# Optimization experiments

Hardware: AMD Instinct MI355X
Metric: run time of the kernel (lower is better)

## Reference

```python
import jax, jax.numpy as jnp
from jax import lax
import numpy as np

K = 2        # k-hop MIS / number of rw SpGEMM iterations
EPS = 0.5    # lazy random-walk epsilon
N = 2048     # nodes
D = 512      # feature dim
E = 65536    # edges (avg degree 32)


def setup_inputs() -> dict:
    key = jax.random.key(0)
    k1, k2, k3, k4 = jax.random.split(key, 4)
    edge_index = jax.random.randint(k1, (2, E), 0, N, dtype=jnp.int32)
    edge_attr = jax.random.uniform(k2, (E,), dtype=jnp.float32)
    x = jax.random.normal(k3, (N, D), dtype=jnp.float32)
    rank = jnp.arange(N, dtype=jnp.int32)  # node ordering ('random' ordering = some permutation; identity here)
    u = jax.random.uniform(k4, (N, N), dtype=jnp.float32)  # noise for row-wise multinomial sampling
    return {"edge_index": edge_index, "edge_attr": edge_attr, "x": x, "rank": rank, "u": u}


def _maximal_k_independent_set(row, col, rank, n, k):
    """Greedy maximal k-independent set: nodes that are local rank-minima within k hops."""
    big = jnp.int32(n)

    def prop_min(r):  # one hop of min-propagation (message row -> col), keep self
        return jnp.minimum(jax.ops.segment_min(r[row], col, num_segments=n), r)

    def prop_or(b):   # one hop of boolean OR propagation (as int32)
        return jnp.maximum(jax.ops.segment_max(b[row], col, num_segments=n), b)

    def cond(st):
        mis, mask, mr = st
        return ~jnp.all(mask)

    def body(st):
        mis, mask, mr = st
        for _ in range(k):
            mr = prop_min(mr)
        mis = mis | (rank == mr)
        mk = mis.astype(jnp.int32)
        for _ in range(k):
            mk = prop_or(mk)
        mask = mk > 0
        mr = jnp.where(mask, big, rank)
        return mis, mask, mr

    init = (jnp.zeros(n, bool), jnp.zeros(n, bool), rank)
    mis, _, _ = lax.while_loop(cond, body, init)
    return mis


def _row_normalize(m):
    s = m.sum(axis=1, keepdims=True)
    return m / jnp.where(s > 0, s, 1.0)


def reference(edge_index, edge_attr, x, rank, u):
    n = x.shape[0]
    row, col = edge_index[0], edge_index[1]

    # --- MIS over the graph structure (integer-only) ---
    mis = _maximal_k_independent_set(row, col, rank, n, K)

    # --- adjacency (dense padded form of the SparseTensor) ---
    adj = jnp.zeros((n, n), x.dtype).at[row, col].add(edge_attr)

    # --- lazy random walk: rw = D^-1 A, offdiag *= (1-eps), diag = old_diag + eps ---
    rw = _row_normalize(adj)
    di = jnp.arange(n)
    new_diag = rw[di, di] + EPS  # computed BEFORE scaling, per original code
    rw = (rw * (1.0 - EPS)).at[di, di].set(new_diag)

    # --- c_mat = rw^K @ eye[:, mis]; padded to [n, n] with zero non-MIS columns ---
    c = jnp.where(mis[None, :], jnp.eye(n, dtype=x.dtype), 0.0)
    for _ in range(K):
        c = rw @ c
    c = _row_normalize(c)

    # --- sample_partition_matrix: per-row multinomial via Gumbel-argmax ---
    g = -jnp.log(-jnp.log(u + 1e-20) + 1e-20)
    logits = jnp.where(c > 0, jnp.log(jnp.maximum(c, 1e-30)), -jnp.inf) + g
    cluster = jnp.argmax(logits, axis=1)                 # [n] cluster id (a MIS column)
    c_hard = jax.nn.one_hot(cluster, n, dtype=x.dtype)   # partition matrix [n, n]

    # --- p_inv = row-normalized c_hard.T ---
    counts = c_hard.sum(axis=0)
    p_inv = c_hard.T / jnp.where(counts > 0, counts, 1.0)[:, None]

    # --- coarsen: c^T A c, pool: p_inv @ x ---
    adj_c = c_hard.T @ adj @ c_hard
    x_pool = p_inv @ x
    return adj_c, c_hard, p_inv, mis, x_pool
```

## Files before the change

kernel.cpp:

```cpp
#include <hip/hip_runtime.h>
#include <hip/hip_bf16.h>
#include <math.h>
#include <stdint.h>

#define NN 2048
#define DD 512
#define EE 65536
#define EPSV 0.5f
#define SEN 2048

static const size_t SZ = (size_t)NN * NN;

__global__ __launch_bounds__(256) void build_adj(const int* __restrict__ row,
                                                 const int* __restrict__ col,
                                                 const float* __restrict__ attr,
                                                 float* __restrict__ adj,
                                                 float* __restrict__ rowsum,
                                                 int* __restrict__ degree,
                                                 int* __restrict__ cdeg) {
  int e = blockIdx.x * 256 + threadIdx.x;
  float a = attr[e];
  int r = row[e], c = col[e];
  atomicAdd(&adj[r * NN + c], a);
  atomicAdd(&rowsum[r], a);
  atomicAdd(&degree[r], 1);
  atomicAdd(&cdeg[c], 1);
}

__global__ __launch_bounds__(1024) void csr_scan_pad(const int* __restrict__ degree,
                                                     const int* __restrict__ cdeg,
                                                     int* __restrict__ row_ptr,
                                                     int* __restrict__ fill_ptr,
                                                     int* __restrict__ col_ptr,
                                                     int* __restrict__ cfill_ptr,
                                                     unsigned short* __restrict__ colidx,
                                                     unsigned short* __restrict__ rowidx) {
  __shared__ int a[NN], b[NN], c[NN], d[NN];
  int t = threadIdx.x;
  for (int v = t; v < NN; v += 1024) {
    a[v] = (degree[v] + 15) & ~15;
    c[v] = (cdeg[v] + 15) & ~15;
  }
  __syncthreads();
  int* s1 = a; int* d1 = b; int* s2 = c; int* d2 = d;
  for (int off = 1; off < NN; off <<= 1) {
    for (int v = t; v < NN; v += 1024) {
      d1[v] = s1[v] + (v >= off ? s1[v - off] : 0);
      d2[v] = s2[v] + (v >= off ? s2[v - off] : 0);
    }
    __syncthreads();
    int* tp = s1; s1 = d1; d1 = tp;
    tp = s2; s2 = d2; d2 = tp;
  }
  for (int v = t; v < NN; v += 1024) {
    int dg = degree[v];
    int end = s1[v];
    int excl = end - ((dg + 15) & ~15);
    row_ptr[v] = excl;
    fill_ptr[v] = excl;
    for (int e = excl + dg; e < end; ++e) colidx[e] = (unsigned short)v;
    dg = cdeg[v];
    end = s2[v];
    excl = end - ((dg + 15) & ~15);
    col_ptr[v] = excl;
    cfill_ptr[v] = excl;
    for (int e = excl + dg; e < end; ++e) rowidx[e] = (unsigned short)v;
  }
  if (t == 0) {
    row_ptr[NN] = s1[NN - 1];
    col_ptr[NN] = s2[NN - 1];
  }
}

__global__ __launch_bounds__(256) void csr_fill(const int* __restrict__ row,
                                                const int* __restrict__ col,
                                                int* __restrict__ fill_ptr,
                                                int* __restrict__ cfill_ptr,
                                                unsigned short* __restrict__ colidx,
                                                unsigned short* __restrict__ rowidx) {
  int e = blockIdx.x * 256 + threadIdx.x;
  int r = row[e], c = col[e];
  colidx[atomicAdd(&fill_ptr[r], 1)] = (unsigned short)c;
  rowidx[atomicAdd(&cfill_ptr[c], 1)] = (unsigned short)r;
}

__global__ __launch_bounds__(1024) void mis_kernel(const int* __restrict__ row_ptr_g,
                                                   const int* __restrict__ col_ptr_g,
                                                   const unsigned short* __restrict__ colidx,
                                                   const unsigned short* __restrict__ rowidx,
                                                   const int* __restrict__ rank_g,
                                                   int* __restrict__ mis_flag,
                                                   int* __restrict__ mis_list,
                                                   int* __restrict__ misinv,
                                                   int* __restrict__ mis_count) {
  __shared__ int rank_s[NN];
  __shared__ int mr[NN];
  __shared__ int cov[NN];
  __shared__ int dly[NN];
  __shared__ int mis_s[NN];
  __shared__ int row_ptr_s[NN + 1];
  __shared__ int col_ptr_s[NN + 1];
  __shared__ int unc[2][NN];
  __shared__ int dl[NN];
  __shared__ int ucnt[2];
  __shared__ int dcnt;
  __shared__ int cnt;
  int t = threadIdx.x;
  const uint4* col4 = (const uint4*)colidx;
  const uint4* row4 = (const uint4*)rowidx;

  for (int v = t; v < NN; v += 1024) {
    int rk = rank_g[v];
    rank_s[v] = rk;
    mr[v] = rk;
    cov[v] = 0;
    dly[v] = 0;
    mis_s[v] = 0;
    row_ptr_s[v] = row_ptr_g[v];
    col_ptr_s[v] = col_ptr_g[v];
    unc[0][v] = v;
  }
  if (t == 0) {
    row_ptr_s[NN] = row_ptr_g[NN];
    col_ptr_s[NN] = col_ptr_g[NN];
    ucnt[0] = NN;
    ucnt[1] = 0;
    dcnt = 0;
    cnt = 0;
  }
  __syncthreads();

  int cur = 0;
  for (int round = 0; round < NN; ++round) {
    int U = ucnt[cur];
    if (round) {
      for (int v = t; v < NN; v += 1024) {
        mr[v] = cov[v] ? SEN : rank_s[v];
        dly[v] = 0;
      }
      if (t == 0) { ucnt[cur ^ 1] = 0; dcnt = 0; }
      __syncthreads();
    }
    for (int i = t; i < U; i += 1024) {
      int v = unc[cur][i];
      int val = rank_s[v];
      int e0 = row_ptr_s[v];
      int nch = (row_ptr_s[v + 1] - e0) >> 3;
      const uint4* b4 = col4 + (e0 >> 3);
      for (int cI = 0; cI < nch; cI += 2) {
        uint4 A = b4[cI], B = b4[cI + 1];
        atomicMin(&mr[A.x & 0xFFFFu], val); atomicMin(&mr[A.x >> 16], val);
        atomicMin(&mr[A.y & 0xFFFFu], val); atomicMin(&mr[A.y >> 16], val);
        atomicMin(&mr[A.z & 0xFFFFu], val); atomicMin(&mr[A.z >> 16], val);
        atomicMin(&mr[A.w & 0xFFFFu], val); atomicMin(&mr[A.w >> 16], val);
        atomicMin(&mr[B.x & 0xFFFFu], val); atomicMin(&mr[B.x >> 16], val);
        atomicMin(&mr[B.y & 0xFFFFu], val); atomicMin(&mr[B.y >> 16], val);
        atomicMin(&mr[B.z & 0xFFFFu], val); atomicMin(&mr[B.z >> 16], val);
        atomicMin(&mr[B.w & 0xFFFFu], val); atomicMin(&mr[B.w >> 16], val);
      }
    }
    __syncthreads();
    for (int i = t; i < U; i += 1024) {
      int v = unc[cur][i];
      int val = mr[v];
      int e0 = col_ptr_s[v];
      int nch = (col_ptr_s[v + 1] - e0) >> 3;
      const uint4* b4 = row4 + (e0 >> 3);
      for (int cI = 0; cI < nch; cI += 2) {
        uint4 A = b4[cI], B = b4[cI + 1];
        int m0 = min(mr[A.x & 0xFFFFu], mr[A.x >> 16]);
        int m1 = min(mr[A.y & 0xFFFFu], mr[A.y >> 16]);
        int m2 = min(mr[A.z & 0xFFFFu], mr[A.z >> 16]);
        int m3 = min(mr[A.w & 0xFFFFu], mr[A.w >> 16]);
        int m4 = min(mr[B.x & 0xFFFFu], mr[B.x >> 16]);
        int m5 = min(mr[B.y & 0xFFFFu], mr[B.y >> 16]);
        int m6 = min(mr[B.z & 0xFFFFu], mr[B.z >> 16]);
        int m7 = min(mr[B.w & 0xFFFFu], mr[B.w >> 16]);
        val = min(val, min(min(min(m0, m1), min(m2, m3)),
                           min(min(m4, m5), min(m6, m7))));
      }
      if (rank_s[v] == val) {
        mis_s[v] = 1;
        dly[v] = 1;
        dl[atomicAdd(&dcnt, 1)] = v;
      }
    }
    __syncthreads();
    int D = dcnt;
    for (int i = t; i < D; i += 1024) {
      int v = dl[i];
      int e0 = row_ptr_s[v];
      int nch = (row_ptr_s[v + 1] - e0) >> 3;
      const uint4* b4 = col4 + (e0 >> 3);
      for (int cI = 0; cI < nch; cI += 2) {
        uint4 A = b4[cI], B = b4[cI + 1];
        dly[A.x & 0xFFFFu] = 1; dly[A.x >> 16] = 1;
        dly[A.y & 0xFFFFu] = 1; dly[A.y >> 16] = 1;
        dly[A.z & 0xFFFFu] = 1; dly[A.z >> 16] = 1;
        dly[A.w & 0xFFFFu] = 1; dly[A.w >> 16] = 1;
        dly[B.x & 0xFFFFu] = 1; dly[B.x >> 16] = 1;
        dly[B.y & 0xFFFFu] = 1; dly[B.y >> 16] = 1;
        dly[B.z & 0xFFFFu] = 1; dly[B.z >> 16] = 1;
        dly[B.w & 0xFFFFu] = 1; dly[B.w >> 16] = 1;
      }
    }
    __syncthreads();
    for (int i = t; i < U; i += 1024) {
      int v = unc[cur][i];
      int c1 = dly[v];
      if (!c1) {
        int e0 = col_ptr_s[v];
        int nch = (col_ptr_s[v + 1] - e0) >> 3;
        const uint4* b4 = row4 + (e0 >> 3);
        for (int cI = 0; cI < nch; cI += 2) {
          uint4 A = b4[cI], B = b4[cI + 1];
          c1 |= dly[A.x & 0xFFFFu] | dly[A.x >> 16] |
                dly[A.y & 0xFFFFu] | dly[A.y >> 16] |
                dly[A.z & 0xFFFFu] | dly[A.z >> 16] |
                dly[A.w & 0xFFFFu] | dly[A.w >> 16] |
                dly[B.x & 0xFFFFu] | dly[B.x >> 16] |
                dly[B.y & 0xFFFFu] | dly[B.y >> 16] |
                dly[B.z & 0xFFFFu] | dly[B.z >> 16] |
                dly[B.w & 0xFFFFu] | dly[B.w >> 16];
          if (c1) break;
        }
      }
      if (c1) cov[v] = 1;
      else unc[cur ^ 1][atomicAdd(&ucnt[cur ^ 1], 1)] = v;
    }
    __syncthreads();
    if (ucnt[cur ^ 1] == 0) break;
    cur ^= 1;
  }

  for (int v = t; v < NN; v += 1024) {
    int s = mis_s[v];
    mis_flag[v] = s;
    int slot = -1;
    if (s) {
      slot = atomicAdd(&cnt, 1);
      mis_list[slot] = v;
    }
    misinv[v] = slot;
  }
  __syncthreads();
  if (t == 0) *mis_count = cnt;
}

__global__ __launch_bounds__(256) void rw_transform_gather(float* __restrict__ adj,
                                                           const float* __restrict__ rowsum,
                                                           const int* __restrict__ misinv,
                                                           float* __restrict__ Bc) {
  int idx = blockIdx.x * 256 + threadIdx.x;
  int i = idx >> 11, j = idx & (NN - 1);
  float s = rowsum[i];
  s = (s > 0.f) ? s : 1.f;
  float v = adj[idx] / s;
  v = (i == j) ? (v + EPSV) : (v * (1.f - EPSV));
  adj[idx] = v;
  int tc = misinv[j];
  if (tc >= 0) Bc[(size_t)tc * NN + i] = v;
}

__device__ inline unsigned int f32_key(float x) {
  unsigned int u = __float_as_uint(x);
  return (u & 0x80000000u) ? ~u : (u | 0x80000000u);
}
__device__ inline float dot4(float4 a, float4 b) {
  return ((a.x * b.x + a.y * b.y) + (a.z * b.z + a.w * b.w));
}
__device__ inline unsigned long long umax64(unsigned long long a, unsigned long long b) {
  return a > b ? a : b;
}

__global__ __launch_bounds__(256) void c2_argmax(const float* __restrict__ rw,
                                                 const float* __restrict__ Bc,
                                                 const float* __restrict__ u,
                                                 const int* __restrict__ mis_list,
                                                 const int* __restrict__ mis_count,
                                                 unsigned long long* __restrict__ packed) {
  int M = *mis_count;
  int ncg = (M + 3) >> 2;
  int njobs = ncg * 64;
  int lane = threadIdx.x & 63, w = threadIdx.x >> 6;
  for (int j = blockIdx.x; j < njobs; j += gridDim.x) {
    int cg = j >> 6, tile = j & 63;
    int c0 = cg * 4;
    float4 creg[4][8];
    int mcol[4];
#pragma unroll
    for (int cc = 0; cc < 4; ++cc) {
      int colv = c0 + cc;
      int cl = colv < M ? colv : (M - 1);
      mcol[cc] = mis_list[cl];
      const float4* cb = (const float4*)(Bc + (size_t)cl * NN);
#pragma unroll
      for (int q = 0; q < 8; ++q) creg[cc][q] = cb[q * 64 + lane];
    }
    int rbase = tile * 32 + w * 8;
#pragma unroll
    for (int it = 0; it < 8; ++it) {
      int r = rbase + it;
      const float4* rp = (const float4*)(rw + (size_t)r * NN);
      float4 a0 = rp[lane], a1 = rp[64 + lane], a2 = rp[128 + lane], a3 = rp[192 + lane];
      float4 a4 = rp[256 + lane], a5 = rp[320 + lane], a6 = rp[384 + lane], a7 = rp[448 + lane];
      float sacc[4];
#pragma unroll
      for (int cc = 0; cc < 4; ++cc) {
        float s01 = dot4(a0, creg[cc][0]) + dot4(a1, creg[cc][1]);
        float s23 = dot4(a2, creg[cc][2]) + dot4(a3, creg[cc][3]);
        float s45 = dot4(a4, creg[cc][4]) + dot4(a5, creg[cc][5]);
        float s67 = dot4(a6, creg[cc][6]) + dot4(a7, creg[cc][7]);
        float s = (s01 + s23) + (s45 + s67);
        s += __shfl_xor(s, 32);
        s += __shfl_xor(s, 16);
        s += __shfl_xor(s, 8);
        s += __shfl_xor(s, 4);
        s += __shfl_xor(s, 2);
        s += __shfl_xor(s, 1);
        sacc[cc] = s;
      }
      if (lane == 0) {
        unsigned long long best = 0ull;
#pragma unroll
        for (int cc = 0; cc < 4; ++cc) {
          if (c0 + cc < M && sacc[cc] > 0.f) {
            int m = mcol[cc];
            float uu = u[(size_t)r * NN + m];
            float g = -logf(-logf(uu + 1e-20f) + 1e-20f);
            float logit = logf(sacc[cc]) + g;
            unsigned long long key =
                ((unsigned long long)f32_key(logit) << 32) | (unsigned int)(NN - 1 - m);
            best = umax64(best, key);
          }
        }
        if (best) atomicMax(&packed[r], best);
      }
    }
  }
}

__global__ __launch_bounds__(256) void cluster_decode(const unsigned long long* __restrict__ packed,
                                                      int* __restrict__ cluster,
                                                      int* __restrict__ counts) {
  int i = blockIdx.x * 256 + threadIdx.x;
  unsigned long long p = packed[i];
  int m = (p == 0ull) ? 0 : (NN - 1 - (int)(p & 0xFFFFFFFFull));
  cluster[i] = m;
  atomicAdd(&counts[m], 1);
}

__global__ __launch_bounds__(256) void scatter_fused(const int* __restrict__ row,
                                                     const int* __restrict__ col,
                                                     const float* __restrict__ attr,
                                                     const float* __restrict__ x,
                                                     const int* __restrict__ cluster,
                                                     float* __restrict__ adjc,
                                                     float* __restrict__ xp) {
  int idx = blockIdx.x * 256 + threadIdx.x;
  if (idx < EE) {
    int cr = cluster[row[idx]], cc = cluster[col[idx]];
    atomicAdd(&adjc[(size_t)cr * NN + cc], attr[idx]);
  }
  int i = idx >> 9;
  atomicAdd(&xp[cluster[i] * DD + (idx & (DD - 1))], x[idx]);
}

__global__ __launch_bounds__(256) void write_chpm(const int* __restrict__ cluster,
                                                  const int* __restrict__ counts,
                                                  const int* __restrict__ mis_flag,
                                                  float* __restrict__ out_ch,
                                                  float* __restrict__ out_pinv,
                                                  float* __restrict__ out_mis,
                                                  float* __restrict__ out_xp) {
  int idx = blockIdx.x * 256 + threadIdx.x;
  int a = idx >> 11, b = idx & (NN - 1);
  out_ch[idx] = (cluster[a] == b) ? 1.f : 0.f;
  float pv = 0.f;
  if (cluster[b] == a) {
    int c = counts[a];
    pv = 1.f / (float)(c > 0 ? c : 1);
  }
  out_pinv[idx] = pv;
  if (idx < NN) out_mis[idx] = mis_flag[idx] ? 1.f : 0.f;
  if (idx < NN * DD) {
    int c = counts[idx >> 9];
    out_xp[idx] = out_xp[idx] / (float)(c > 0 ? c : 1);
  }
}

extern "C" void kernel_launch(void* const* d_in, const int* in_sizes, int n_in,
                              void* d_out, int out_size, void* d_ws, size_t ws_size,
                              hipStream_t stream) {
  const int*   edge_index = (const int*)d_in[0];
  const float* edge_attr  = (const float*)d_in[1];
  const float* x          = (const float*)d_in[2];
  const int*   rank       = (const int*)d_in[3];
  const float* u          = (const float*)d_in[4];
  float* out              = (float*)d_out;

  const int* row = edge_index;
  const int* col = edge_index + EE;

  float* out_adjc = out;
  float* out_ch   = out + SZ;
  float* out_pinv = out + 2 * SZ;
  float* out_mis  = out + 3 * SZ;
  float* out_xp   = out + 3 * SZ + NN;

  unsigned long long* packed = (unsigned long long*)d_ws;
  float* rowsum    = (float*)(packed + NN);
  int*   counts    = (int*)(rowsum + NN);
  int*   degree    = counts + NN;
  int*   cdeg      = degree + NN;
  int*   mis_flag  = cdeg + NN;
  int*   cluster   = mis_flag + NN;
  int*   mis_list  = cluster + NN;
  int*   misinv    = mis_list + NN;
  int*   mis_count = misinv + NN;
  int*   fill_ptr  = mis_count + 1;
  int*   cfill_ptr = fill_ptr + NN;
  int*   row_ptr   = cfill_ptr + NN;
  int*   col_ptr   = row_ptr + NN + 1;
  unsigned short* colidx =
      (unsigned short*)(((uintptr_t)(col_ptr + NN + 1) + 31) & ~(uintptr_t)31);
  unsigned short* rowidx = colidx + 98304;

  hipMemsetAsync(out_adjc, 0, SZ * sizeof(float), stream);
  hipMemsetAsync(out_xp, 0, (size_t)NN * DD * sizeof(float), stream);
  hipMemsetAsync(d_ws, 0, NN * sizeof(unsigned long long) + 4 * NN * sizeof(int), stream);

  build_adj<<<EE / 256, 256, 0, stream>>>(row, col, edge_attr, out_adjc, rowsum, degree, cdeg);
  csr_scan_pad<<<1, 1024, 0, stream>>>(degree, cdeg, row_ptr, fill_ptr, col_ptr, cfill_ptr,
                                       colidx, rowidx);
  csr_fill<<<EE / 256, 256, 0, stream>>>(row, col, fill_ptr, cfill_ptr, colidx, rowidx);
  mis_kernel<<<1, 1024, 0, stream>>>(row_ptr, col_ptr, colidx, rowidx, rank,
                                     mis_flag, mis_list, misinv, mis_count);
  rw_transform_gather<<<(NN * NN) / 256, 256, 0, stream>>>(out_adjc, rowsum, misinv, out_ch);
  c2_argmax<<<1024, 256, 0, stream>>>(out_adjc, out_ch, u, mis_list, mis_count, packed);
  cluster_decode<<<NN / 256, 256, 0, stream>>>(packed, cluster, counts);

  hipMemsetAsync(out_adjc, 0, SZ * sizeof(float), stream);
  scatter_fused<<<(NN * DD) / 256, 256, 0, stream>>>(row, col, edge_attr, x, cluster,
                                                     out_adjc, out_xp);

  write_chpm<<<(NN * NN) / 256, 256, 0, stream>>>(cluster, counts, mis_flag,
                                                  out_ch, out_pinv, out_mis, out_xp);
}
```

Measured before the change: 265.2 us.

## Fuse CSR construction into MIS kernel and fold small launches into neighbors

Moves degree counting, rowsum, prefix scan and CSR fill into the single-block MIS kernel using shared-memory atomics, which drops the csr_scan_pad and csr_fill launches and two memsets. The mark-neighbors step is merged into the MIS-detection loop, removing a barrier and the dl list. cluster_decode is folded into scatter_fused, and the x_pool zeroing moves into rw_transform_gather. The cost is that the edge scatter now runs on one 1024-thread workgroup instead of the whole GPU, and the kernel needs a 64-entry per-thread register array.

```diff
diff --git a/kernel.cpp b/kernel.cpp
--- a/kernel.cpp
+++ b/kernel.cpp
@@ -8,91 +8,26 @@
 #define EE 65536
 #define EPSV 0.5f
 #define SEN 2048
+#define PADE 98304
 
 static const size_t SZ = (size_t)NN * NN;
 
 __global__ __launch_bounds__(256) void build_adj(const int* __restrict__ row,
                                                  const int* __restrict__ col,
                                                  const float* __restrict__ attr,
-                                                 float* __restrict__ adj,
-                                                 float* __restrict__ rowsum,
-                                                 int* __restrict__ degree,
-                                                 int* __restrict__ cdeg) {
+                                                 float* __restrict__ adj) {
   int e = blockIdx.x * 256 + threadIdx.x;
-  float a = attr[e];
-  int r = row[e], c = col[e];
-  atomicAdd(&adj[r * NN + c], a);
-  atomicAdd(&rowsum[r], a);
-  atomicAdd(&degree[r], 1);
-  atomicAdd(&cdeg[c], 1);
-}
-
-__global__ __launch_bounds__(1024) void csr_scan_pad(const int* __restrict__ degree,
-                                                     const int* __restrict__ cdeg,
-                                                     int* __restrict__ row_ptr,
-                                                     int* __restrict__ fill_ptr,
-                                                     int* __restrict__ col_ptr,
-                                                     int* __restrict__ cfill_ptr,
-                                                     unsigned short* __restrict__ colidx,
-                                                     unsigned short* __restrict__ rowidx) {
-  __shared__ int a[NN], b[NN], c[NN], d[NN];
-  int t = threadIdx.x;
-  for (int v = t; v < NN; v += 1024) {
-    a[v] = (degree[v] + 15) & ~15;
-    c[v] = (cdeg[v] + 15) & ~15;
-  }
-  __syncthreads();
-  int* s1 = a; int* d1 = b; int* s2 = c; int* d2 = d;
-  for (int off = 1; off < NN; off <<= 1) {
-    for (int v = t; v < NN; v += 1024) {
-      d1[v] = s1[v] + (v >= off ? s1[v - off] : 0);
-      d2[v] = s2[v] + (v >= off ? s2[v - off] : 0);
-    }
-    __syncthreads();
-    int* tp = s1; s1 = d1; d1 = tp;
-    tp = s2; s2 = d2; d2 = tp;
-  }
-  for (int v = t; v < NN; v += 1024) {
-    int dg = degree[v];
-    int end = s1[v];
-    int excl = end - ((dg + 15) & ~15);
-    row_ptr[v] = excl;
-    fill_ptr[v] = excl;
-    for (int e = excl + dg; e < end; ++e) colidx[e] = (unsigned short)v;
-    dg = cdeg[v];
-    end = s2[v];
-    excl = end - ((dg + 15) & ~15);
-    col_ptr[v] = excl;
-    cfill_ptr[v] = excl;
-    for (int e = excl + dg; e < end; ++e) rowidx[e] = (unsigned short)v;
-  }
-  if (t == 0) {
-    row_ptr[NN] = s1[NN - 1];
-    col_ptr[NN] = s2[NN - 1];
-  }
-}
-
-__global__ __launch_bounds__(256) void csr_fill(const int* __restrict__ row,
-                                                const int* __restrict__ col,
-                                                int* __restrict__ fill_ptr,
-                                                int* __restrict__ cfill_ptr,
-                                                unsigned short* __restrict__ colidx,
-                                                unsigned short* __restrict__ rowidx) {
-  int e = blockIdx.x * 256 + threadIdx.x;
-  int r = row[e], c = col[e];
-  colidx[atomicAdd(&fill_ptr[r], 1)] = (unsigned short)c;
-  rowidx[atomicAdd(&cfill_ptr[c], 1)] = (unsigned short)r;
-}
-
-__global__ __launch_bounds__(1024) void mis_kernel(const int* __restrict__ row_ptr_g,
-                                                   const int* __restrict__ col_ptr_g,
-                                                   const unsigned short* __restrict__ colidx,
-                                                   const unsigned short* __restrict__ rowidx,
-                                                   const int* __restrict__ rank_g,
-                                                   int* __restrict__ mis_flag,
-                                                   int* __restrict__ mis_list,
-                                                   int* __restrict__ misinv,
-                                                   int* __restrict__ mis_count) {
+  atomicAdd(&adj[row[e] * NN + col[e]], attr[e]);
+}
+
+__global__ __launch_bounds__(1024) void fused_mis(
+    const int* __restrict__ row, const int* __restrict__ col,
+    const float* __restrict__ attr, const int* __restrict__ rank_g,
+    unsigned short* __restrict__ colidx, unsigned short* __restrict__ rowidx,
+    float* __restrict__ rowsum_g, unsigned long long* __restrict__ packed,
+    int* __restrict__ counts, int* __restrict__ mis_flag,
+    int* __restrict__ mis_list, int* __restrict__ misinv,
+    int* __restrict__ mis_count) {
   __shared__ int rank_s[NN];
   __shared__ int mr[NN];
   __shared__ int cov[NN];
@@ -101,13 +36,77 @@
   __shared__ int row_ptr_s[NN + 1];
   __shared__ int col_ptr_s[NN + 1];
   __shared__ int unc[2][NN];
-  __shared__ int dl[NN];
   __shared__ int ucnt[2];
-  __shared__ int dcnt;
   __shared__ int cnt;
   int t = threadIdx.x;
-  const uint4* col4 = (const uint4*)colidx;
-  const uint4* row4 = (const uint4*)rowidx;
+  float* rowsum_s = (float*)mis_s;
+
+  for (int v = t; v < NN; v += 1024) {
+    mr[v] = 0;
+    cov[v] = 0;
+    rowsum_s[v] = 0.f;
+  }
+  __syncthreads();
+  unsigned pe[64];
+#pragma unroll
+  for (int i = 0; i < 64; ++i) {
+    int e = t + 1024 * i;
+    int r = row[e], c = col[e];
+    pe[i] = ((unsigned)r << 11) | (unsigned)c;
+    atomicAdd(&mr[r], 1);
+    atomicAdd(&cov[c], 1);
+    atomicAdd(&rowsum_s[r], attr[e]);
+  }
+  __syncthreads();
+
+  int* s1 = dly;    int* d1 = mis_s;
+  int* s2 = unc[0]; int* d2 = unc[1];
+  for (int v = t; v < NN; v += 1024) {
+    rowsum_g[v] = rowsum_s[v];
+    s1[v] = (mr[v] + 15) & ~15;
+    s2[v] = (cov[v] + 15) & ~15;
+  }
+  __syncthreads();
+  for (int off = 1; off < NN; off <<= 1) {
+    for (int v = t; v < NN; v += 1024) {
+      d1[v] = s1[v] + (v >= off ? s1[v - off] : 0);
+      d2[v] = s2[v] + (v >= off ? s2[v - off] : 0);
+    }
+    __syncthreads();
+    int* tp = s1; s1 = d1; d1 = tp;
+    tp = s2; s2 = d2; d2 = tp;
+  }
+  for (int v = t; v < NN; v += 1024) {
+    int end = s1[v];
+    row_ptr_s[v] = end - ((mr[v] + 15) & ~15);
+    end = s2[v];
+    col_ptr_s[v] = end - ((cov[v] + 15) & ~15);
+  }
+  if (t == 0) {
+    row_ptr_s[NN] = s1[NN - 1];
+    col_ptr_s[NN] = s2[NN - 1];
+  }
+  __syncthreads();
+
+  for (int v = t; v < NN; v += 1024) {
+    int e0 = row_ptr_s[v];
+    dly[v] = e0;
+    for (int e = e0 + mr[v]; e < row_ptr_s[v + 1]; ++e)
+      colidx[e] = (unsigned short)v;
+    e0 = col_ptr_s[v];
+    mis_s[v] = e0;
+    for (int e = e0 + cov[v]; e < col_ptr_s[v + 1]; ++e)
+      rowidx[e] = (unsigned short)v;
+  }
+  __syncthreads();
+#pragma unroll
+  for (int i = 0; i < 64; ++i) {
+    unsigned p = pe[i];
+    int r = p >> 11, c = p & 2047;
+    colidx[atomicAdd(&dly[r], 1)] = (unsigned short)c;
+    rowidx[atomicAdd(&mis_s[c], 1)] = (unsigned short)r;
+  }
+  __syncthreads();
 
   for (int v = t; v < NN; v += 1024) {
     int rk = rank_g[v];
@@ -116,19 +115,19 @@
     cov[v] = 0;
     dly[v] = 0;
     mis_s[v] = 0;
-    row_ptr_s[v] = row_ptr_g[v];
-    col_ptr_s[v] = col_ptr_g[v];
     unc[0][v] = v;
+    packed[v] = 0ull;
+    counts[v] = 0;
   }
   if (t == 0) {
-    row_ptr_s[NN] = row_ptr_g[NN];
-    col_ptr_s[NN] = col_ptr_g[NN];
     ucnt[0] = NN;
     ucnt[1] = 0;
-    dcnt = 0;
     cnt = 0;
   }
   __syncthreads();
+
+  const uint4* col4 = (const uint4*)colidx;
+  const uint4* row4 = (const uint4*)rowidx;
 
   int cur = 0;
   for (int round = 0; round < NN; ++round) {
@@ -138,7 +137,7 @@
         mr[v] = cov[v] ? SEN : rank_s[v];
         dly[v] = 0;
       }
-      if (t == 0) { ucnt[cur ^ 1] = 0; dcnt = 0; }
+      if (t == 0) ucnt[cur ^ 1] = 0;
       __syncthreads();
     }
     for (int i = t; i < U; i += 1024) {
@@ -182,26 +181,20 @@
       if (rank_s[v] == val) {
         mis_s[v] = 1;
         dly[v] = 1;
-        dl[atomicAdd(&dcnt, 1)] = v;
-      }
-    }
-    __syncthreads();
-    int D = dcnt;
-    for (int i = t; i < D; i += 1024) {
-      int v = dl[i];
-      int e0 = row_ptr_s[v];
-      int nch = (row_ptr_s[v + 1] - e0) >> 3;
-      const uint4* b4 = col4 + (e0 >> 3);
-      for (int cI = 0; cI < nch; cI += 2) {
-        uint4 A = b4[cI], B = b4[cI + 1];
-        dly[A.x & 0xFFFFu] = 1; dly[A.x >> 16] = 1;
-        dly[A.y & 0xFFFFu] = 1; dly[A.y >> 16] = 1;
-        dly[A.z & 0xFFFFu] = 1; dly[A.z >> 16] = 1;
-        dly[A.w & 0xFFFFu] = 1; dly[A.w >> 16] = 1;
-        dly[B.x & 0xFFFFu] = 1; dly[B.x >> 16] = 1;
-        dly[B.y & 0xFFFFu] = 1; dly[B.y >> 16] = 1;
-        dly[B.z & 0xFFFFu] = 1; dly[B.z >> 16] = 1;
-        dly[B.w & 0xFFFFu] = 1; dly[B.w >> 16] = 1;
+        int f0 = row_ptr_s[v];
+        int fch = (row_ptr_s[v + 1] - f0) >> 3;
+        const uint4* c4 = col4 + (f0 >> 3);
+        for (int cI = 0; cI < fch; cI += 2) {
+          uint4 A = c4[cI], B = c4[cI + 1];
+          dly[A.x & 0xFFFFu] = 1; dly[A.x >> 16] = 1;
+          dly[A.y & 0xFFFFu] = 1; dly[A.y >> 16] = 1;
+          dly[A.z & 0xFFFFu] = 1; dly[A.z >> 16] = 1;
+          dly[A.w & 0xFFFFu] = 1; dly[A.w >> 16] = 1;
+          dly[B.x & 0xFFFFu] = 1; dly[B.x >> 16] = 1;
+          dly[B.y & 0xFFFFu] = 1; dly[B.y >> 16] = 1;
+          dly[B.z & 0xFFFFu] = 1; dly[B.z >> 16] = 1;
+          dly[B.w & 0xFFFFu] = 1; dly[B.w >> 16] = 1;
+        }
       }
     }
     __syncthreads();
@@ -250,7 +243,8 @@
 __global__ __launch_bounds__(256) void rw_transform_gather(float* __restrict__ adj,
                                                            const float* __restrict__ rowsum,
                                                            const int* __restrict__ misinv,
-                                                           float* __restrict__ Bc) {
+                                                           float* __restrict__ Bc,
+                                                           float* __restrict__ out_xp) {
   int idx = blockIdx.x * 256 + threadIdx.x;
   int i = idx >> 11, j = idx & (NN - 1);
   float s = rowsum[i];
@@ -260,6 +254,7 @@
   adj[idx] = v;
   int tc = misinv[j];
   if (tc >= 0) Bc[(size_t)tc * NN + i] = v;
+  if (idx < NN * DD) out_xp[idx] = 0.f;
 }
 
 __device__ inline unsigned int f32_key(float x) {
@@ -271,6 +266,9 @@
 }
 __device__ inline unsigned long long umax64(unsigned long long a, unsigned long long b) {
   return a > b ? a : b;
+}
+__device__ inline int pdecode(unsigned long long p) {
+  return (p == 0ull) ? 0 : (NN - 1 - (int)(p & 0xFFFFFFFFull));
 }
 
 __global__ __launch_bounds__(256) void c2_argmax(const float* __restrict__ rw,
@@ -340,30 +338,28 @@
   }
 }
 
-__global__ __launch_bounds__(256) void cluster_decode(const unsigned long long* __restrict__ packed,
-                                                      int* __restrict__ cluster,
-                                                      int* __restrict__ counts) {
-  int i = blockIdx.x * 256 + threadIdx.x;
-  unsigned long long p = packed[i];
-  int m = (p == 0ull) ? 0 : (NN - 1 - (int)(p & 0xFFFFFFFFull));
-  cluster[i] = m;
-  atomicAdd(&counts[m], 1);
-}
-
 __global__ __launch_bounds__(256) void scatter_fused(const int* __restrict__ row,
                                                      const int* __restrict__ col,
                                                      const float* __restrict__ attr,
                                                      const float* __restrict__ x,
-                                                     const int* __restrict__ cluster,
+                                                     const unsigned long long* __restrict__ packed,
+                                                     int* __restrict__ cluster,
+                                                     int* __restrict__ counts,
                                                      float* __restrict__ adjc,
                                                      float* __restrict__ xp) {
   int idx = blockIdx.x * 256 + threadIdx.x;
+  int i = idx >> 9;
+  int ci = pdecode(packed[i]);
+  if ((idx & 511) == 0) {
+    cluster[i] = ci;
+    atomicAdd(&counts[ci], 1);
+  }
   if (idx < EE) {
-    int cr = cluster[row[idx]], cc = cluster[col[idx]];
+    int cr = pdecode(packed[row[idx]]);
+    int cc = pdecode(packed[col[idx]]);
     atomicAdd(&adjc[(size_t)cr * NN + cc], attr[idx]);
   }
-  int i = idx >> 9;
-  atomicAdd(&xp[cluster[i] * DD + (idx & (DD - 1))], x[idx]);
+  atomicAdd(&xp[ci * DD + (idx & (DD - 1))], x[idx]);
 }
 
 __global__ __launch_bounds__(256) void write_chpm(const int* __restrict__ cluster,
@@ -411,38 +407,27 @@
   unsigned long long* packed = (unsigned long long*)d_ws;
   float* rowsum    = (float*)(packed + NN);
   int*   counts    = (int*)(rowsum + NN);
-  int*   degree    = counts + NN;
-  int*   cdeg      = degree + NN;
-  int*   mis_flag  = cdeg + NN;
+  int*   mis_flag  = counts + NN;
   int*   cluster   = mis_flag + NN;
   int*   mis_list  = cluster + NN;
   int*   misinv    = mis_list + NN;
   int*   mis_count = misinv + NN;
-  int*   fill_ptr  = mis_count + 1;
-  int*   cfill_ptr = fill_ptr + NN;
-  int*   row_ptr   = cfill_ptr + NN;
-  int*   col_ptr   = row_ptr + NN + 1;
   unsigned short* colidx =
-      (unsigned short*)(((uintptr_t)(col_ptr + NN + 1) + 31) & ~(uintptr_t)31);
-  unsigned short* rowidx = colidx + 98304;
+      (unsigned short*)(((uintptr_t)(mis_count + 1) + 31) & ~(uintptr_t)31);
+  unsigned short* rowidx = colidx + PADE;
 
   hipMemsetAsync(out_adjc, 0, SZ * sizeof(float), stream);
-  hipMemsetAsync(out_xp, 0, (size_t)NN * DD * sizeof(float), stream);
-  hipMemsetAsync(d_ws, 0, NN * sizeof(unsigned long long) + 4 * NN * sizeof(int), stream);
-
-  build_adj<<<EE / 256, 256, 0, stream>>>(row, col, edge_attr, out_adjc, rowsum, degree, cdeg);
-  csr_scan_pad<<<1, 1024, 0, stream>>>(degree, cdeg, row_ptr, fill_ptr, col_ptr, cfill_ptr,
-                                       colidx, rowidx);
-  csr_fill<<<EE / 256, 256, 0, stream>>>(row, col, fill_ptr, cfill_ptr, colidx, rowidx);
-  mis_kernel<<<1, 1024, 0, stream>>>(row_ptr, col_ptr, colidx, rowidx, rank,
-                                     mis_flag, mis_list, misinv, mis_count);
-  rw_transform_gather<<<(NN * NN) / 256, 256, 0, stream>>>(out_adjc, rowsum, misinv, out_ch);
+  build_adj<<<EE / 256, 256, 0, stream>>>(row, col, edge_attr, out_adjc);
+  fused_mis<<<1, 1024, 0, stream>>>(row, col, edge_attr, rank, colidx, rowidx,
+                                    rowsum, packed, counts, mis_flag, mis_list,
+                                    misinv, mis_count);
+  rw_transform_gather<<<(NN * NN) / 256, 256, 0, stream>>>(out_adjc, rowsum, misinv,
+                                                           out_ch, out_xp);
   c2_argmax<<<1024, 256, 0, stream>>>(out_adjc, out_ch, u, mis_list, mis_count, packed);
-  cluster_decode<<<NN / 256, 256, 0, stream>>>(packed, cluster, counts);
 
   hipMemsetAsync(out_adjc, 0, SZ * sizeof(float), stream);
-  scatter_fused<<<(NN * DD) / 256, 256, 0, stream>>>(row, col, edge_attr, x, cluster,
-                                                     out_adjc, out_xp);
+  scatter_fused<<<(NN * DD) / 256, 256, 0, stream>>>(row, col, edge_attr, x, packed,
+                                                     cluster, counts, out_adjc, out_xp);
 
   write_chpm<<<(NN * NN) / 256, 256, 0, stream>>>(cluster, counts, mis_flag,
                                                   out_ch, out_pinv, out_mis, out_xp);
```

After: 414.8 us. 1.56x slower.

## Build random-walk rows from CSR and fuse zeroing, decode and scatter kernels

Applied to the files above, without the earlier changes.

The dense adjacency is no longer built with global atomics on a zeroed 16MB buffer. Edge values are stored alongside the CSR column indices, and each row of the random-walk matrix is built in shared memory, then written once. Several memsets and small kernels are merged: the cluster decode is combined with zeroing the output, and the pooled-feature and coarsened-adjacency scatters are folded into the one-hot/p_inv writer, with pooled features divided by cluster counts before the atomic add. This removes two full-matrix memsets and one full-matrix pass, at the cost of shared-memory atomics per row and a changed summation order for x_pool.

```diff
diff --git a/kernel.cpp b/kernel.cpp
--- a/kernel.cpp
+++ b/kernel.cpp
@@ -8,23 +8,17 @@
 #define EE 65536
 #define EPSV 0.5f
 #define SEN 2048
+#define PADE 98304
 
 static const size_t SZ = (size_t)NN * NN;
 
-__global__ __launch_bounds__(256) void build_adj(const int* __restrict__ row,
+__global__ __launch_bounds__(256) void count_deg(const int* __restrict__ row,
                                                  const int* __restrict__ col,
-                                                 const float* __restrict__ attr,
-                                                 float* __restrict__ adj,
-                                                 float* __restrict__ rowsum,
                                                  int* __restrict__ degree,
                                                  int* __restrict__ cdeg) {
   int e = blockIdx.x * 256 + threadIdx.x;
-  float a = attr[e];
-  int r = row[e], c = col[e];
-  atomicAdd(&adj[r * NN + c], a);
-  atomicAdd(&rowsum[r], a);
-  atomicAdd(&degree[r], 1);
-  atomicAdd(&cdeg[c], 1);
+  atomicAdd(&degree[row[e]], 1);
+  atomicAdd(&cdeg[col[e]], 1);
 }
 
 __global__ __launch_bounds__(1024) void csr_scan_pad(const int* __restrict__ degree,
@@ -34,12 +28,17 @@
                                                      int* __restrict__ col_ptr,
                                                      int* __restrict__ cfill_ptr,
                                                      unsigned short* __restrict__ colidx,
-                                                     unsigned short* __restrict__ rowidx) {
+                                                     unsigned short* __restrict__ rowidx,
+                                                     float* __restrict__ avals,
+                                                     unsigned long long* __restrict__ packed,
+                                                     int* __restrict__ counts) {
   __shared__ int a[NN], b[NN], c[NN], d[NN];
   int t = threadIdx.x;
   for (int v = t; v < NN; v += 1024) {
     a[v] = (degree[v] + 15) & ~15;
     c[v] = (cdeg[v] + 15) & ~15;
+    packed[v] = 0ull;
+    counts[v] = 0;
   }
   __syncthreads();
   int* s1 = a; int* d1 = b; int* s2 = c; int* d2 = d;
@@ -58,7 +57,10 @@
     int excl = end - ((dg + 15) & ~15);
     row_ptr[v] = excl;
     fill_ptr[v] = excl;
-    for (int e = excl + dg; e < end; ++e) colidx[e] = (unsigned short)v;
+    for (int e = excl + dg; e < end; ++e) {
+      colidx[e] = (unsigned short)v;
+      avals[e] = 0.f;
+    }
     dg = cdeg[v];
     end = s2[v];
     excl = end - ((dg + 15) & ~15);
@@ -74,13 +76,17 @@
 
 __global__ __launch_bounds__(256) void csr_fill(const int* __restrict__ row,
                                                 const int* __restrict__ col,
+                                                const float* __restrict__ attr,
                                                 int* __restrict__ fill_ptr,
                                                 int* __restrict__ cfill_ptr,
                                                 unsigned short* __restrict__ colidx,
-                                                unsigned short* __restrict__ rowidx) {
+                                                unsigned short* __restrict__ rowidx,
+                                                float* __restrict__ avals) {
   int e = blockIdx.x * 256 + threadIdx.x;
   int r = row[e], c = col[e];
-  colidx[atomicAdd(&fill_ptr[r], 1)] = (unsigned short)c;
+  int pos = atomicAdd(&fill_ptr[r], 1);
+  colidx[pos] = (unsigned short)c;
+  avals[pos] = attr[e];
   rowidx[atomicAdd(&cfill_ptr[c], 1)] = (unsigned short)r;
 }
 
@@ -247,19 +253,38 @@
   if (t == 0) *mis_count = cnt;
 }
 
-__global__ __launch_bounds__(256) void rw_transform_gather(float* __restrict__ adj,
-                                                           const float* __restrict__ rowsum,
-                                                           const int* __restrict__ misinv,
-                                                           float* __restrict__ Bc) {
-  int idx = blockIdx.x * 256 + threadIdx.x;
-  int i = idx >> 11, j = idx & (NN - 1);
-  float s = rowsum[i];
+__global__ __launch_bounds__(256) void rw_build(const int* __restrict__ row_ptr,
+                                                const unsigned short* __restrict__ colidx,
+                                                const float* __restrict__ avals,
+                                                const int* __restrict__ misinv,
+                                                float* __restrict__ rw,
+                                                float* __restrict__ Bc) {
+  int i = blockIdx.x;
+  __shared__ float rowbuf[NN];
+  __shared__ float ssum;
+  int t = threadIdx.x;
+  for (int j = t; j < NN; j += 256) rowbuf[j] = 0.f;
+  if (t == 0) ssum = 0.f;
+  __syncthreads();
+  int e0 = row_ptr[i], e1 = row_ptr[i + 1];
+  float part = 0.f;
+  for (int e = e0 + t; e < e1; e += 256) {
+    float a = avals[e];
+    atomicAdd(&rowbuf[colidx[e]], a);
+    part += a;
+  }
+  for (int off = 32; off; off >>= 1) part += __shfl_down(part, off);
+  if ((t & 63) == 0) atomicAdd(&ssum, part);
+  __syncthreads();
+  float s = ssum;
   s = (s > 0.f) ? s : 1.f;
-  float v = adj[idx] / s;
-  v = (i == j) ? (v + EPSV) : (v * (1.f - EPSV));
-  adj[idx] = v;
-  int tc = misinv[j];
-  if (tc >= 0) Bc[(size_t)tc * NN + i] = v;
+  for (int j = t; j < NN; j += 256) {
+    float v = rowbuf[j] / s;
+    v = (i == j) ? (v + EPSV) : (v * (1.f - EPSV));
+    rw[(size_t)i * NN + j] = v;
+    int tc = misinv[j];
+    if (tc >= 0) Bc[(size_t)tc * NN + i] = v;
+  }
 }
 
 __device__ inline unsigned int f32_key(float x) {
@@ -271,6 +296,9 @@
 }
 __device__ inline unsigned long long umax64(unsigned long long a, unsigned long long b) {
   return a > b ? a : b;
+}
+__device__ inline int pdecode(unsigned long long p) {
+  return (p == 0ull) ? 0 : (NN - 1 - (int)(p & 0xFFFFFFFFull));
 }
 
 __global__ __launch_bounds__(256) void c2_argmax(const float* __restrict__ rw,
@@ -340,39 +368,33 @@
   }
 }
 
-__global__ __launch_bounds__(256) void cluster_decode(const unsigned long long* __restrict__ packed,
-                                                      int* __restrict__ cluster,
-                                                      int* __restrict__ counts) {
-  int i = blockIdx.x * 256 + threadIdx.x;
-  unsigned long long p = packed[i];
-  int m = (p == 0ull) ? 0 : (NN - 1 - (int)(p & 0xFFFFFFFFull));
-  cluster[i] = m;
-  atomicAdd(&counts[m], 1);
-}
-
-__global__ __launch_bounds__(256) void scatter_fused(const int* __restrict__ row,
-                                                     const int* __restrict__ col,
-                                                     const float* __restrict__ attr,
-                                                     const float* __restrict__ x,
-                                                     const int* __restrict__ cluster,
-                                                     float* __restrict__ adjc,
-                                                     float* __restrict__ xp) {
+__global__ __launch_bounds__(256) void decode_zero(const unsigned long long* __restrict__ packed,
+                                                   int* __restrict__ cluster,
+                                                   int* __restrict__ counts,
+                                                   float* __restrict__ adjc,
+                                                   float* __restrict__ xp) {
   int idx = blockIdx.x * 256 + threadIdx.x;
-  if (idx < EE) {
-    int cr = cluster[row[idx]], cc = cluster[col[idx]];
-    atomicAdd(&adjc[(size_t)cr * NN + cc], attr[idx]);
-  }
-  int i = idx >> 9;
-  atomicAdd(&xp[cluster[i] * DD + (idx & (DD - 1))], x[idx]);
-}
-
-__global__ __launch_bounds__(256) void write_chpm(const int* __restrict__ cluster,
-                                                  const int* __restrict__ counts,
-                                                  const int* __restrict__ mis_flag,
-                                                  float* __restrict__ out_ch,
-                                                  float* __restrict__ out_pinv,
-                                                  float* __restrict__ out_mis,
-                                                  float* __restrict__ out_xp) {
+  if (idx < (int)SZ) adjc[idx] = 0.f;
+  else xp[idx - (int)SZ] = 0.f;
+  if (idx < NN) {
+    int m = pdecode(packed[idx]);
+    cluster[idx] = m;
+    atomicAdd(&counts[m], 1);
+  }
+}
+
+__global__ __launch_bounds__(256) void scatter_chpm(const int* __restrict__ row,
+                                                    const int* __restrict__ col,
+                                                    const float* __restrict__ attr,
+                                                    const float* __restrict__ x,
+                                                    const int* __restrict__ cluster,
+                                                    const int* __restrict__ counts,
+                                                    const int* __restrict__ mis_flag,
+                                                    float* __restrict__ out_ch,
+                                                    float* __restrict__ out_pinv,
+                                                    float* __restrict__ out_mis,
+                                                    float* __restrict__ adjc,
+                                                    float* __restrict__ xp) {
   int idx = blockIdx.x * 256 + threadIdx.x;
   int a = idx >> 11, b = idx & (NN - 1);
   out_ch[idx] = (cluster[a] == b) ? 1.f : 0.f;
@@ -384,8 +406,13 @@
   out_pinv[idx] = pv;
   if (idx < NN) out_mis[idx] = mis_flag[idx] ? 1.f : 0.f;
   if (idx < NN * DD) {
-    int c = counts[idx >> 9];
-    out_xp[idx] = out_xp[idx] / (float)(c > 0 ? c : 1);
+    int i = idx >> 9;
+    int ci = cluster[i];
+    int c = counts[ci];
+    atomicAdd(&xp[ci * DD + (idx & (DD - 1))], x[idx] / (float)(c > 0 ? c : 1));
+  }
+  if (idx < EE) {
+    atomicAdd(&adjc[(size_t)cluster[row[idx]] * NN + cluster[col[idx]]], attr[idx]);
   }
 }
 
@@ -408,12 +435,11 @@
   float* out_mis  = out + 3 * SZ;
   float* out_xp   = out + 3 * SZ + NN;
 
-  unsigned long long* packed = (unsigned long long*)d_ws;
-  float* rowsum    = (float*)(packed + NN);
-  int*   counts    = (int*)(rowsum + NN);
-  int*   degree    = counts + NN;
+  int*   degree    = (int*)d_ws;
   int*   cdeg      = degree + NN;
-  int*   mis_flag  = cdeg + NN;
+  unsigned long long* packed = (unsigned long long*)(cdeg + NN);
+  int*   counts    = (int*)(packed + NN);
+  int*   mis_flag  = counts + NN;
   int*   cluster   = mis_flag + NN;
   int*   mis_list  = cluster + NN;
   int*   misinv    = mis_list + NN;
@@ -424,26 +450,22 @@
   int*   col_ptr   = row_ptr + NN + 1;
   unsigned short* colidx =
       (unsigned short*)(((uintptr_t)(col_ptr + NN + 1) + 31) & ~(uintptr_t)31);
-  unsigned short* rowidx = colidx + 98304;
-
-  hipMemsetAsync(out_adjc, 0, SZ * sizeof(float), stream);
-  hipMemsetAsync(out_xp, 0, (size_t)NN * DD * sizeof(float), stream);
-  hipMemsetAsync(d_ws, 0, NN * sizeof(unsigned long long) + 4 * NN * sizeof(int), stream);
-
-  build_adj<<<EE / 256, 256, 0, stream>>>(row, col, edge_attr, out_adjc, rowsum, degree, cdeg);
-  csr_scan_pad<<<1, 1024, 0, stream>>>(degree, cdeg, row_ptr, fill_ptr, col_ptr, cfill_ptr,
-                                       colidx, rowidx);
-  csr_fill<<<EE / 256, 256, 0, stream>>>(row, col, fill_ptr, cfill_ptr, colidx, rowidx);
+  unsigned short* rowidx = colidx + PADE;
+  float* avals = (float*)(rowidx + PADE);
+
+  hipMemsetAsync(d_ws, 0, 2 * NN * sizeof(int), stream);
+  count_deg<<<EE / 256, 256, 0, stream>>>(row, col, degree, cdeg);
+  csr_scan_pad<<<1, 1024, 0, stream>>>(degree, cdeg, row_ptr, fill_ptr, col_ptr,
+                                       cfill_ptr, colidx, rowidx, avals, packed, counts);
+  csr_fill<<<EE / 256, 256, 0, stream>>>(row, col, edge_attr, fill_ptr, cfill_ptr,
+                                         colidx, rowidx, avals);
   mis_kernel<<<1, 1024, 0, stream>>>(row_ptr, col_ptr, colidx, rowidx, rank,
                                      mis_flag, mis_list, misinv, mis_count);
-  rw_transform_gather<<<(NN * NN) / 256, 256, 0, stream>>>(out_adjc, rowsum, misinv, out_ch);
+  rw_build<<<NN, 256, 0, stream>>>(row_ptr, colidx, avals, misinv, out_adjc, out_ch);
   c2_argmax<<<1024, 256, 0, stream>>>(out_adjc, out_ch, u, mis_list, mis_count, packed);
-  cluster_decode<<<NN / 256, 256, 0, stream>>>(packed, cluster, counts);
-
-  hipMemsetAsync(out_adjc, 0, SZ * sizeof(float), stream);
-  scatter_fused<<<(NN * DD) / 256, 256, 0, stream>>>(row, col, edge_attr, x, cluster,
-                                                     out_adjc, out_xp);
-
-  write_chpm<<<(NN * NN) / 256, 256, 0, stream>>>(cluster, counts, mis_flag,
-                                                  out_ch, out_pinv, out_mis, out_xp);
-}
+  decode_zero<<<(unsigned)((SZ + (size_t)NN * DD) / 256), 256, 0, stream>>>(
+      packed, cluster, counts, out_adjc, out_xp);
+  scatter_chpm<<<(NN * NN) / 256, 256, 0, stream>>>(row, col, edge_attr, x, cluster,
+                                                    counts, mis_flag, out_ch, out_pinv,
+                                                    out_mis, out_adjc, out_xp);
+}
```

Result: faster. 247.0 us, median of 2 (-6.8%).
